# Kernel optimization log

Measured on AMD Instinct MI355X. Metric: run time of the kernel, lower is better.

The kernel has to match this reference:

```python
import jax, jax.numpy as jnp
import numpy as np

VOCAB = 10000
N_STATE = 384
N_HEAD = 6
N_CTX = 448
B = 128
T = 448  # seq len, must be <= N_CTX


def setup_inputs() -> dict:
    key = jax.random.key(0)
    ks = jax.random.split(key, 10)
    def w(k, shape, scale=0.02):
        return jax.random.normal(k, shape, dtype=jnp.float32) * scale
    return {
        "x": jax.random.randint(ks[0], (B, T), 0, VOCAB),
        "emb": w(ks[1], (VOCAB, N_STATE)),
        "Wq": w(ks[2], (N_STATE, N_STATE)), "bq": w(ks[3], (N_STATE,)),
        "Wk": w(ks[4], (N_STATE, N_STATE)),  # key layer has no bias
        "Wv": w(ks[5], (N_STATE, N_STATE)), "bv": w(ks[6], (N_STATE,)),
        "Wo": w(ks[7], (N_STATE, N_STATE)), "bo": w(ks[8], (N_STATE,)),
    }


def reference(x, emb, Wq, bq, Wk, Wv, bv, Wo, bo):
    b, t = x.shape
    d = N_STATE // N_HEAD  # 64
    scale = d ** (-0.25)

    h = emb[x]                          # [b, t, n_state] embedding lookup
    q = h @ Wq.T + bq                   # [b, t, n_state]
    k = h @ Wk.T                        # key linear has no bias
    v = h @ Wv.T + bv

    # split heads: [b, t, H, d]
    qh = q.reshape(b, t, N_HEAD, d) * scale
    kh = k.reshape(b, t, N_HEAD, d) * scale
    vh = v.reshape(b, t, N_HEAD, d)

    qk = jnp.einsum('bqhd,bkhd->bhqk', qh, kh)          # [b, H, t, t]
    mask = jnp.triu(jnp.full((t, t), -jnp.inf, dtype=qk.dtype), 1)
    qk = qk + mask                                      # causal mask add
    w = jax.nn.softmax(qk.astype(jnp.float32), axis=-1).astype(q.dtype)

    wv = jnp.einsum('bhqk,bkhd->bqhd', w, vh).reshape(b, t, N_STATE)
    out = wv @ Wo.T + bo
    return (out, k, v)
```

## Files before the change

kernel.cpp:

```cpp
#include <hip/hip_runtime.h>
#include <hip/hip_bf16.h>
#include <stdint.h>

typedef __bf16 bf16x8 __attribute__((ext_vector_type(8)));
typedef short short8v __attribute__((ext_vector_type(8)));
typedef float f32x4 __attribute__((ext_vector_type(4)));

#define B_     128
#define T_     448
#define NS     384
#define NH     6
#define HD     64
#define VOCAB_ 10000
#define NOUT   22020096

#define OFF_WQ   0
#define OFF_WK   147456
#define OFF_WV   294912
#define OFF_WO   442368
#define OFF_QTAB 589824
#define OFF_KTAB 4429824
#define OFF_VTAB 8269824
#define OFF_CTX  12109824

#define NATT (B_ * NH * 7)
#define NGAT 10752
#define NFUSE (NATT * 3)

__device__ __forceinline__ unsigned short f2bf(float f) {
    union { __bf16 h; unsigned short u; } v;
    v.h = (__bf16)f;
    return v.u;
}
__device__ __forceinline__ float bf2f(unsigned short u) {
    union { uint32_t u; float f; } v; v.u = (uint32_t)u << 16;
    return v.f;
}

__global__ __launch_bounds__(256) void k_prep(
    const float* __restrict__ Wq, const float* __restrict__ Wk,
    const float* __restrict__ Wv, const float* __restrict__ Wo,
    unsigned short* __restrict__ ws)
{
    const float* srcs[4] = {Wq, Wk, Wv, Wo};
    const int seg = blockIdx.y;
    int i = (blockIdx.x * 256 + threadIdx.x) * 4;
    if (i >= 147456) return;
    float4 v = *(const float4*)(srcs[seg] + i);
    ushort4 o;
    o.x = f2bf(v.x); o.y = f2bf(v.y); o.z = f2bf(v.z); o.w = f2bf(v.w);
    *(ushort4*)(ws + seg * 147456 + i) = o;
}

__global__ __launch_bounds__(256) void k_table(
    const float* __restrict__ emb, const unsigned short* __restrict__ ws,
    const float* __restrict__ bq, const float* __restrict__ bv,
    unsigned short* __restrict__ wso)
{
    const int p  = blockIdx.y;
    const int v0 = blockIdx.x * 32;
    const int tid = threadIdx.x;
    const int lane = tid & 63, wv = tid >> 6;

    __shared__ __align__(16) unsigned short sA[32][392];

    {
        int r = tid >> 3;
        int srow = min(v0 + r, VOCAB_ - 1);
        const float* src = emb + (size_t)srow * NS + (tid & 7) * 48;
        unsigned short* dst = &sA[r][(tid & 7) * 48];
        #pragma unroll
        for (int j = 0; j < 6; ++j) {
            float4 a0 = *(const float4*)(src + j * 8);
            float4 a1 = *(const float4*)(src + j * 8 + 4);
            ushort4 o0, o1;
            o0.x = f2bf(a0.x); o0.y = f2bf(a0.y); o0.z = f2bf(a0.z); o0.w = f2bf(a0.w);
            o1.x = f2bf(a1.x); o1.y = f2bf(a1.y); o1.z = f2bf(a1.z); o1.w = f2bf(a1.w);
            *(ushort4*)(dst + j * 8) = o0;
            *(ushort4*)(dst + j * 8 + 4) = o1;
        }
    }
    __syncthreads();

    f32x4 acc[2][6];
    #pragma unroll
    for (int i = 0; i < 2; ++i)
        #pragma unroll
        for (int j = 0; j < 6; ++j) acc[i][j] = (f32x4){0.f, 0.f, 0.f, 0.f};

    const int colA = lane & 15;
    const int kb = (lane >> 4) * 8;
    const unsigned short* wlane =
        ws + (size_t)p * 147456 + (size_t)(wv * 96 + colA) * NS + kb;

    #pragma unroll 2
    for (int kc = 0; kc < 12; ++kc) {
        bf16x8 a[2], b[6];
        #pragma unroll
        for (int mf = 0; mf < 2; ++mf)
            a[mf] = *(const bf16x8*)&sA[mf * 16 + colA][kc * 32 + kb];
        #pragma unroll
        for (int nf = 0; nf < 6; ++nf)
            b[nf] = *(const bf16x8*)(wlane + (size_t)(nf * 16) * NS + kc * 32);
        #pragma unroll
        for (int mf = 0; mf < 2; ++mf)
            #pragma unroll
            for (int nf = 0; nf < 6; ++nf)
                acc[mf][nf] = __builtin_amdgcn_mfma_f32_16x16x32_bf16(
                    a[mf], b[nf], acc[mf][nf], 0, 0, 0);
    }

    const int r0 = (lane >> 4) * 4;
    const float scale = 0.35355339059327373f;
    const float qscale = 0.35355339059327373f * 1.4426950408889634f;

    if (p == 0) {
        unsigned short* qt_ = wso + OFF_QTAB;
        #pragma unroll
        for (int nf = 0; nf < 6; ++nf) {
            int n = wv * 96 + nf * 16 + colA;
            float bias = bq[n];
            #pragma unroll
            for (int mf = 0; mf < 2; ++mf)
                #pragma unroll
                for (int r = 0; r < 4; ++r) {
                    int row = v0 + mf * 16 + r0 + r;
                    if (row < VOCAB_)
                        qt_[(size_t)row * NS + n] = f2bf((acc[mf][nf][r] + bias) * qscale);
                }
        }
    } else if (p == 1) {
        unsigned short* kt_ = wso + OFF_KTAB;
        #pragma unroll
        for (int nf = 0; nf < 6; ++nf) {
            int n = wv * 96 + nf * 16 + colA;
            #pragma unroll
            for (int mf = 0; mf < 2; ++mf)
                #pragma unroll
                for (int r = 0; r < 4; ++r) {
                    int row = v0 + mf * 16 + r0 + r;
                    if (row < VOCAB_)
                        kt_[(size_t)row * NS + n] = f2bf(acc[mf][nf][r] * scale);
                }
        }
    } else {
        unsigned short* vt_ = wso + OFF_VTAB;
        #pragma unroll
        for (int nf = 0; nf < 6; ++nf) {
            int n = wv * 96 + nf * 16 + colA;
            float bias = bv[n];
            #pragma unroll
            for (int mf = 0; mf < 2; ++mf)
                #pragma unroll
                for (int r = 0; r < 4; ++r) {
                    int row = v0 + mf * 16 + r0 + r;
                    if (row < VOCAB_)
                        vt_[(size_t)row * NS + n] = f2bf(acc[mf][nf][r] + bias);
                }
        }
    }
}

__global__ __launch_bounds__(256) void k_attn_gather(
    const int* __restrict__ x, const unsigned short* __restrict__ ws,
    unsigned short* __restrict__ ctxb,
    float* __restrict__ out_k, float* __restrict__ out_v)
{
    const int swz = (blockIdx.x & 7) * (NFUSE / 8) + (blockIdx.x >> 3);
    const int r3 = swz % 3;
    const int q3 = swz / 3;

    if (r3 != 0) {
        int i = (2 * q3 + (r3 - 1)) * 256 + threadIdx.x;
        int row = i / 48;
        int c = (i - row * 48) * 8;
        int tok = x[row];
        const unsigned short* ks = ws + OFF_KTAB + (size_t)tok * NS + c;
        const unsigned short* vs = ws + OFF_VTAB + (size_t)tok * NS + c;
        ushort4 k0 = *(const ushort4*)ks;
        ushort4 k1 = *(const ushort4*)(ks + 4);
        ushort4 v0 = *(const ushort4*)vs;
        ushort4 v1 = *(const ushort4*)(vs + 4);
        const float inv = 2.8284271247461903f;
        float4 fk0 = {bf2f(k0.x) * inv, bf2f(k0.y) * inv, bf2f(k0.z) * inv, bf2f(k0.w) * inv};
        float4 fk1 = {bf2f(k1.x) * inv, bf2f(k1.y) * inv, bf2f(k1.z) * inv, bf2f(k1.w) * inv};
        float4 fv0 = {bf2f(v0.x), bf2f(v0.y), bf2f(v0.z), bf2f(v0.w)};
        float4 fv1 = {bf2f(v1.x), bf2f(v1.y), bf2f(v1.z), bf2f(v1.w)};
        size_t base = (size_t)row * NS + c;
        *(float4*)(out_k + base)     = fk0;
        *(float4*)(out_k + base + 4) = fk1;
        *(float4*)(out_v + base)     = fv0;
        *(float4*)(out_v + base + 4) = fv1;
        return;
    }

    const int bid = q3;
    const int qt = bid % 7;
    const int h  = (bid / 7) % NH;
    const int b  = bid / (7 * NH);
    const int tid = threadIdx.x;
    const int lane = tid & 63, wv = tid >> 6;

    __shared__ __align__(16) unsigned short sK[64][72];
    __shared__ __align__(16) unsigned short sVT[64][72];
    __shared__ __align__(16) unsigned short sP[4][16][72];

    const int* xb = x + (size_t)b * T_;
    const unsigned short* qtab = ws + OFF_QTAB;
    const unsigned short* ktab = ws + OFF_KTAB;
    const unsigned short* vtab = ws + OFF_VTAB;

    const int qrow = qt * 64 + wv * 16 + (lane & 15);
    const int qtok = xb[qrow];
    const unsigned short* qbase =
        qtab + (size_t)qtok * NS + h * HD + (lane >> 4) * 8;
    bf16x8 qf0 = *(const bf16x8*)qbase;
    bf16x8 qf1 = *(const bf16x8*)(qbase + 32);

    f32x4 o[4];
    #pragma unroll
    for (int nf = 0; nf < 4; ++nf) o[nf] = (f32x4){0.f, 0.f, 0.f, 0.f};
    float lsum[4] = {0.f, 0.f, 0.f, 0.f};

    const int tk = tid >> 2;
    const int cc = (tid & 3) * 16;
    const int vd = tid & 63;
    const int vg = tid >> 6;

    short8v kr0, kr1;
    unsigned short tv[16];
    {
        int tkn = xb[tk];
        const unsigned short* kset = ktab + (size_t)tkn * NS + h * HD + cc;
        kr0 = *(const short8v*)kset;
        kr1 = *(const short8v*)(kset + 8);
        #pragma unroll
        for (int j = 0; j < 16; ++j) {
            int t = xb[vg * 16 + j];
            tv[j] = vtab[(size_t)t * NS + h * HD + vd];
        }
    }

    for (int kv = 0; kv <= qt; ++kv) {
        __syncthreads();
        *(short8v*)&sK[tk][cc]           = kr0;
        *(short8v*)&sK[tk][cc + 8]       = kr1;
        *(short8v*)&sVT[vd][vg * 16]     = *(const short8v*)&tv[0];
        *(short8v*)&sVT[vd][vg * 16 + 8] = *(const short8v*)&tv[8];
        __syncthreads();

        if (kv < qt) {
            int base = (kv + 1) * 64;
            int tkn = xb[base + tk];
            const unsigned short* kset = ktab + (size_t)tkn * NS + h * HD + cc;
            kr0 = *(const short8v*)kset;
            kr1 = *(const short8v*)(kset + 8);
            #pragma unroll
            for (int j = 0; j < 16; ++j) {
                int t = xb[base + vg * 16 + j];
                tv[j] = vtab[(size_t)t * NS + h * HD + vd];
            }
        }

        f32x4 s[4];
        #pragma unroll
        for (int nf = 0; nf < 4; ++nf) s[nf] = (f32x4){0.f, 0.f, 0.f, 0.f};
        #pragma unroll
        for (int nf = 0; nf < 4; ++nf) {
            bf16x8 kb0 = *(const bf16x8*)&sK[nf * 16 + (lane & 15)][(lane >> 4) * 8];
            s[nf] = __builtin_amdgcn_mfma_f32_16x16x32_bf16(qf0, kb0, s[nf], 0, 0, 0);
            bf16x8 kb1 = *(const bf16x8*)&sK[nf * 16 + (lane & 15)][32 + (lane >> 4) * 8];
            s[nf] = __builtin_amdgcn_mfma_f32_16x16x32_bf16(qf1, kb1, s[nf], 0, 0, 0);
        }

        if (kv == qt) {
            const int rloc = wv * 16 + (lane >> 4) * 4;
            const int cloc = lane & 15;
            #pragma unroll
            for (int nf = 0; nf < 4; ++nf)
                #pragma unroll
                for (int r = 0; r < 4; ++r) {
                    float sv = (cloc + nf * 16 > rloc + r) ? -1e30f : s[nf][r];
                    float p = exp2f(sv);
                    s[nf][r] = p;
                    lsum[r] += p;
                }
        } else {
            #pragma unroll
            for (int nf = 0; nf < 4; ++nf)
                #pragma unroll
                for (int r = 0; r < 4; ++r) {
                    float p = exp2f(s[nf][r]);
                    s[nf][r] = p;
                    lsum[r] += p;
                }
        }

        #pragma unroll
        for (int nf = 0; nf < 4; ++nf)
            #pragma unroll
            for (int r = 0; r < 4; ++r)
                sP[wv][(lane >> 4) * 4 + r][nf * 16 + (lane & 15)] = f2bf(s[nf][r]);
        asm volatile("s_waitcnt lgkmcnt(0)" ::: "memory");

        bf16x8 pa0 = *(const bf16x8*)&sP[wv][lane & 15][(lane >> 4) * 8];
        bf16x8 pa1 = *(const bf16x8*)&sP[wv][lane & 15][32 + (lane >> 4) * 8];
        #pragma unroll
        for (int nf = 0; nf < 4; ++nf) {
            bf16x8 vb0 = *(const bf16x8*)&sVT[nf * 16 + (lane & 15)][(lane >> 4) * 8];
            o[nf] = __builtin_amdgcn_mfma_f32_16x16x32_bf16(pa0, vb0, o[nf], 0, 0, 0);
            bf16x8 vb1 = *(const bf16x8*)&sVT[nf * 16 + (lane & 15)][32 + (lane >> 4) * 8];
            o[nf] = __builtin_amdgcn_mfma_f32_16x16x32_bf16(pa1, vb1, o[nf], 0, 0, 0);
        }
    }

    float inv[4];
    #pragma unroll
    for (int r = 0; r < 4; ++r) {
        float l = lsum[r];
        #pragma unroll
        for (int off = 1; off < 16; off <<= 1)
            l += __shfl_xor(l, off, 16);
        inv[r] = 1.0f / l;
    }

    #pragma unroll
    for (int nf = 0; nf < 4; ++nf) {
        int col = h * HD + nf * 16 + (lane & 15);
        #pragma unroll
        for (int r = 0; r < 4; ++r) {
            int rowg = qt * 64 + wv * 16 + (lane >> 4) * 4 + r;
            ctxb[((size_t)b * T_ + rowg) * NS + col] = f2bf(o[nf][r] * inv[r]);
        }
    }
}

__global__ __launch_bounds__(256) void k_oproj(
    const unsigned short* __restrict__ ws, const float* __restrict__ bo,
    float* __restrict__ out)
{
    const int m0 = blockIdx.x * 64;
    const int tid = threadIdx.x;
    const int lane = tid & 63, wv = tid >> 6;

    __shared__ __align__(16) unsigned short sA[64][392];

    const unsigned short* ctxb = ws + OFF_CTX;

    {
        int r = tid >> 2, seg = tid & 3;
        const unsigned short* src = ctxb + (size_t)(m0 + r) * NS + seg * 96;
        unsigned short* dst = &sA[r][seg * 96];
        #pragma unroll
        for (int j = 0; j < 12; ++j)
            *(short8v*)(dst + j * 8) = *(const short8v*)(src + j * 8);
    }
    __syncthreads();

    f32x4 acc[4][6];
    #pragma unroll
    for (int i = 0; i < 4; ++i)
        #pragma unroll
        for (int j = 0; j < 6; ++j) acc[i][j] = (f32x4){0.f, 0.f, 0.f, 0.f};

    const int colA = lane & 15;
    const int kb = (lane >> 4) * 8;
    const unsigned short* wlane =
        ws + OFF_WO + (size_t)(wv * 96 + colA) * NS + kb;

    #pragma unroll 2
    for (int kc = 0; kc < 12; ++kc) {
        bf16x8 a[4], bfr[6];
        #pragma unroll
        for (int mf = 0; mf < 4; ++mf)
            a[mf] = *(const bf16x8*)&sA[mf * 16 + colA][kc * 32 + kb];
        #pragma unroll
        for (int nf = 0; nf < 6; ++nf)
            bfr[nf] = *(const bf16x8*)(wlane + (size_t)(nf * 16) * NS + kc * 32);
        #pragma unroll
        for (int mf = 0; mf < 4; ++mf)
            #pragma unroll
            for (int nf = 0; nf < 6; ++nf)
                acc[mf][nf] = __builtin_amdgcn_mfma_f32_16x16x32_bf16(
                    a[mf], bfr[nf], acc[mf][nf], 0, 0, 0);
    }

    const int r0 = (lane >> 4) * 4;
    #pragma unroll
    for (int nf = 0; nf < 6; ++nf) {
        int n = wv * 96 + nf * 16 + colA;
        float bias = bo[n];
        #pragma unroll
        for (int mf = 0; mf < 4; ++mf)
            #pragma unroll
            for (int r = 0; r < 4; ++r)
                out[(size_t)(m0 + mf * 16 + r0 + r) * NS + n] = acc[mf][nf][r] + bias;
    }
}

extern "C" void kernel_launch(void* const* d_in, const int* in_sizes, int n_in,
                              void* d_out, int out_size, void* d_ws, size_t ws_size,
                              hipStream_t stream) {
    const int*   x   = (const int*)d_in[0];
    const float* emb = (const float*)d_in[1];
    const float* Wq  = (const float*)d_in[2];
    const float* bq  = (const float*)d_in[3];
    const float* Wk  = (const float*)d_in[4];
    const float* Wv  = (const float*)d_in[5];
    const float* bv  = (const float*)d_in[6];
    const float* Wo  = (const float*)d_in[7];
    const float* bo  = (const float*)d_in[8];

    float* out   = (float*)d_out;
    float* out_k = out + NOUT;
    float* out_v = out + 2 * (size_t)NOUT;
    unsigned short* ws = (unsigned short*)d_ws;

    k_prep<<<dim3(144, 4), 256, 0, stream>>>(Wq, Wk, Wv, Wo, ws);
    k_table<<<dim3(313, 3), 256, 0, stream>>>(emb, ws, bq, bv, ws);
    k_attn_gather<<<dim3(NFUSE), 256, 0, stream>>>(x, ws, ws + OFF_CTX,
                                                   out_k, out_v);
    k_oproj<<<dim3(896), 256, 0, stream>>>(ws, bo, out);
}
```

Baseline: 192.9 us.

## Fuse output projection into attention blocks looping over all heads

Each attention block now handles one batch and query tile across all six heads sequentially. It writes the normalized context into shared memory and then runs the Wo projection directly. This removes the bf16 context round-trip through global memory and the separate oproj launch. The cost is far fewer attention blocks (896 instead of 5376) doing longer serial work, plus about 50KB more shared memory per block, which can reduce occupancy and load balance. Query tiles are now scheduled longest-first.

```diff
diff --git a/kernel.cpp b/kernel.cpp
--- a/kernel.cpp
+++ b/kernel.cpp
@@ -21,11 +21,10 @@
 #define OFF_QTAB 589824
 #define OFF_KTAB 4429824
 #define OFF_VTAB 8269824
-#define OFF_CTX  12109824
-
-#define NATT (B_ * NH * 7)
-#define NGAT 10752
-#define NFUSE (NATT * 3)
+
+#define NATT2  896
+#define NGAT   10752
+#define NFUSE  (NATT2 + NGAT)
 
 __device__ __forceinline__ unsigned short f2bf(float f) {
     union { __bf16 h; unsigned short u; } v;
@@ -161,17 +160,18 @@
     }
 }
 
-__global__ __launch_bounds__(256) void k_attn_gather(
+__global__ __launch_bounds__(256) void k_fused(
     const int* __restrict__ x, const unsigned short* __restrict__ ws,
-    unsigned short* __restrict__ ctxb,
+    const float* __restrict__ bo, float* __restrict__ out,
     float* __restrict__ out_k, float* __restrict__ out_v)
 {
-    const int swz = (blockIdx.x & 7) * (NFUSE / 8) + (blockIdx.x >> 3);
-    const int r3 = swz % 3;
-    const int q3 = swz / 3;
-
-    if (r3 != 0) {
-        int i = (2 * q3 + (r3 - 1)) * 256 + threadIdx.x;
+    const int gid = blockIdx.x;
+    const int tid = threadIdx.x;
+
+    if (gid >= NATT2) {
+        int g = gid - NATT2;
+        int cs = (g & 7) * (NGAT / 8) + (g >> 3);
+        int i = cs * 256 + tid;
         int row = i / 48;
         int c = (i - row * 48) * 8;
         int tok = x[row];
@@ -194,16 +194,15 @@
         return;
     }
 
-    const int bid = q3;
-    const int qt = bid % 7;
-    const int h  = (bid / 7) % NH;
-    const int b  = bid / (7 * NH);
-    const int tid = threadIdx.x;
+    const int as = (gid & 7) * (NATT2 / 8) + (gid >> 3);
+    const int b  = as / 7;
+    const int qt = 6 - (as % 7);
     const int lane = tid & 63, wv = tid >> 6;
 
     __shared__ __align__(16) unsigned short sK[64][72];
     __shared__ __align__(16) unsigned short sVT[64][72];
     __shared__ __align__(16) unsigned short sP[4][16][72];
+    __shared__ __align__(16) unsigned short sO[64][392];
 
     const int* xb = x + (size_t)b * T_;
     const unsigned short* qtab = ws + OFF_QTAB;
@@ -212,15 +211,12 @@
 
     const int qrow = qt * 64 + wv * 16 + (lane & 15);
     const int qtok = xb[qrow];
-    const unsigned short* qbase =
-        qtab + (size_t)qtok * NS + h * HD + (lane >> 4) * 8;
-    bf16x8 qf0 = *(const bf16x8*)qbase;
-    bf16x8 qf1 = *(const bf16x8*)(qbase + 32);
 
     f32x4 o[4];
     #pragma unroll
     for (int nf = 0; nf < 4; ++nf) o[nf] = (f32x4){0.f, 0.f, 0.f, 0.f};
     float lsum[4] = {0.f, 0.f, 0.f, 0.f};
+    bf16x8 qf0, qf1;
 
     const int tk = tid >> 2;
     const int cc = (tid & 3) * 16;
@@ -231,17 +227,19 @@
     unsigned short tv[16];
     {
         int tkn = xb[tk];
-        const unsigned short* kset = ktab + (size_t)tkn * NS + h * HD + cc;
+        const unsigned short* kset = ktab + (size_t)tkn * NS + cc;
         kr0 = *(const short8v*)kset;
         kr1 = *(const short8v*)(kset + 8);
         #pragma unroll
         for (int j = 0; j < 16; ++j) {
             int t = xb[vg * 16 + j];
-            tv[j] = vtab[(size_t)t * NS + h * HD + vd];
-        }
-    }
-
-    for (int kv = 0; kv <= qt; ++kv) {
+            tv[j] = vtab[(size_t)t * NS + vd];
+        }
+    }
+
+    int h = 0, kv = 0;
+    const int NT = NH * (qt + 1);
+    for (int t = 0; t < NT; ++t) {
         __syncthreads();
         *(short8v*)&sK[tk][cc]           = kr0;
         *(short8v*)&sK[tk][cc + 8]       = kr1;
@@ -249,17 +247,28 @@
         *(short8v*)&sVT[vd][vg * 16 + 8] = *(const short8v*)&tv[8];
         __syncthreads();
 
-        if (kv < qt) {
-            int base = (kv + 1) * 64;
-            int tkn = xb[base + tk];
-            const unsigned short* kset = ktab + (size_t)tkn * NS + h * HD + cc;
-            kr0 = *(const short8v*)kset;
-            kr1 = *(const short8v*)(kset + 8);
-            #pragma unroll
-            for (int j = 0; j < 16; ++j) {
-                int t = xb[base + vg * 16 + j];
-                tv[j] = vtab[(size_t)t * NS + h * HD + vd];
+        {
+            int nh = h, nkv = kv + 1;
+            if (nkv > qt) { nkv = 0; nh++; }
+            if (nh < NH) {
+                int base = nkv * 64;
+                int tkn = xb[base + tk];
+                const unsigned short* kset = ktab + (size_t)tkn * NS + nh * HD + cc;
+                kr0 = *(const short8v*)kset;
+                kr1 = *(const short8v*)(kset + 8);
+                #pragma unroll
+                for (int j = 0; j < 16; ++j) {
+                    int tt = xb[base + vg * 16 + j];
+                    tv[j] = vtab[(size_t)tt * NS + nh * HD + vd];
+                }
             }
+        }
+
+        if (kv == 0) {
+            const unsigned short* qbase =
+                qtab + (size_t)qtok * NS + h * HD + (lane >> 4) * 8;
+            qf0 = *(const bf16x8*)qbase;
+            qf1 = *(const bf16x8*)(qbase + 32);
         }
 
         f32x4 s[4];
@@ -312,49 +321,34 @@
             bf16x8 vb1 = *(const bf16x8*)&sVT[nf * 16 + (lane & 15)][32 + (lane >> 4) * 8];
             o[nf] = __builtin_amdgcn_mfma_f32_16x16x32_bf16(pa1, vb1, o[nf], 0, 0, 0);
         }
-    }
-
-    float inv[4];
-    #pragma unroll
-    for (int r = 0; r < 4; ++r) {
-        float l = lsum[r];
-        #pragma unroll
-        for (int off = 1; off < 16; off <<= 1)
-            l += __shfl_xor(l, off, 16);
-        inv[r] = 1.0f / l;
-    }
-
-    #pragma unroll
-    for (int nf = 0; nf < 4; ++nf) {
-        int col = h * HD + nf * 16 + (lane & 15);
-        #pragma unroll
-        for (int r = 0; r < 4; ++r) {
-            int rowg = qt * 64 + wv * 16 + (lane >> 4) * 4 + r;
-            ctxb[((size_t)b * T_ + rowg) * NS + col] = f2bf(o[nf][r] * inv[r]);
-        }
-    }
-}
-
-__global__ __launch_bounds__(256) void k_oproj(
-    const unsigned short* __restrict__ ws, const float* __restrict__ bo,
-    float* __restrict__ out)
-{
-    const int m0 = blockIdx.x * 64;
-    const int tid = threadIdx.x;
-    const int lane = tid & 63, wv = tid >> 6;
-
-    __shared__ __align__(16) unsigned short sA[64][392];
-
-    const unsigned short* ctxb = ws + OFF_CTX;
-
-    {
-        int r = tid >> 2, seg = tid & 3;
-        const unsigned short* src = ctxb + (size_t)(m0 + r) * NS + seg * 96;
-        unsigned short* dst = &sA[r][seg * 96];
-        #pragma unroll
-        for (int j = 0; j < 12; ++j)
-            *(short8v*)(dst + j * 8) = *(const short8v*)(src + j * 8);
-    }
+
+        if (kv == qt) {
+            float inv[4];
+            #pragma unroll
+            for (int r = 0; r < 4; ++r) {
+                float l = lsum[r];
+                #pragma unroll
+                for (int off = 1; off < 16; off <<= 1)
+                    l += __shfl_xor(l, off, 16);
+                inv[r] = 1.0f / l;
+            }
+            #pragma unroll
+            for (int nf = 0; nf < 4; ++nf) {
+                int col = h * HD + nf * 16 + (lane & 15);
+                #pragma unroll
+                for (int r = 0; r < 4; ++r)
+                    sO[wv * 16 + (lane >> 4) * 4 + r][col] = f2bf(o[nf][r] * inv[r]);
+            }
+            #pragma unroll
+            for (int nf = 0; nf < 4; ++nf) o[nf] = (f32x4){0.f, 0.f, 0.f, 0.f};
+            #pragma unroll
+            for (int r = 0; r < 4; ++r) lsum[r] = 0.f;
+            h++; kv = 0;
+        } else {
+            kv++;
+        }
+    }
+
     __syncthreads();
 
     f32x4 acc[4][6];
@@ -373,7 +367,7 @@
         bf16x8 a[4], bfr[6];
         #pragma unroll
         for (int mf = 0; mf < 4; ++mf)
-            a[mf] = *(const bf16x8*)&sA[mf * 16 + colA][kc * 32 + kb];
+            a[mf] = *(const bf16x8*)&sO[mf * 16 + colA][kc * 32 + kb];
         #pragma unroll
         for (int nf = 0; nf < 6; ++nf)
             bfr[nf] = *(const bf16x8*)(wlane + (size_t)(nf * 16) * NS + kc * 32);
@@ -385,6 +379,7 @@
                     a[mf], bfr[nf], acc[mf][nf], 0, 0, 0);
     }
 
+    const int m0 = b * T_ + qt * 64;
     const int r0 = (lane >> 4) * 4;
     #pragma unroll
     for (int nf = 0; nf < 6; ++nf) {
@@ -418,7 +413,5 @@
 
     k_prep<<<dim3(144, 4), 256, 0, stream>>>(Wq, Wk, Wv, Wo, ws);
     k_table<<<dim3(313, 3), 256, 0, stream>>>(emb, ws, bq, bv, ws);
-    k_attn_gather<<<dim3(NFUSE), 256, 0, stream>>>(x, ws, ws + OFF_CTX,
-                                                   out_k, out_v);
-    k_oproj<<<dim3(896), 256, 0, stream>>>(ws, bo, out);
-}
+    k_fused<<<dim3(NFUSE), 256, 0, stream>>>(x, ws, bo, out, out_k, out_v);
+}
```

After: 293.7 us. +52.3%, slower.

## Split gather from attention and materialize contiguous bf16 K/V buffers

Applied to the files above, without the earlier changes.

The fused attention+gather kernel becomes two kernels. The gather kernel now also writes bf16 K and V into per-batch contiguous buffers, and the attention kernel reads those buffers directly instead of doing indirect token-indexed lookups into the vocab tables. This removes the dependent index loads and scattered reads from the attention inner loop. The cost is an extra kernel launch, roughly 45 MB of additional bf16 writes and reads, and the loss of overlap between gather and attention work.

```diff
diff --git a/kernel.cpp b/kernel.cpp
--- a/kernel.cpp
+++ b/kernel.cpp
@@ -21,11 +21,12 @@
 #define OFF_QTAB 589824
 #define OFF_KTAB 4429824
 #define OFF_VTAB 8269824
-#define OFF_CTX  12109824
+#define OFF_KB   12109824
+#define OFF_VB   34129920
+#define OFF_CTX  56150016
 
 #define NATT (B_ * NH * 7)
 #define NGAT 10752
-#define NFUSE (NATT * 3)
 
 __device__ __forceinline__ unsigned short f2bf(float f) {
     union { __bf16 h; unsigned short u; } v;
@@ -161,43 +162,45 @@
     }
 }
 
-__global__ __launch_bounds__(256) void k_attn_gather(
+__global__ __launch_bounds__(256) void k_gather(
     const int* __restrict__ x, const unsigned short* __restrict__ ws,
-    unsigned short* __restrict__ ctxb,
-    float* __restrict__ out_k, float* __restrict__ out_v)
+    float* __restrict__ out_k, float* __restrict__ out_v,
+    unsigned short* __restrict__ kbuf, unsigned short* __restrict__ vbuf)
 {
-    const int swz = (blockIdx.x & 7) * (NFUSE / 8) + (blockIdx.x >> 3);
-    const int r3 = swz % 3;
-    const int q3 = swz / 3;
-
-    if (r3 != 0) {
-        int i = (2 * q3 + (r3 - 1)) * 256 + threadIdx.x;
-        int row = i / 48;
-        int c = (i - row * 48) * 8;
-        int tok = x[row];
-        const unsigned short* ks = ws + OFF_KTAB + (size_t)tok * NS + c;
-        const unsigned short* vs = ws + OFF_VTAB + (size_t)tok * NS + c;
-        ushort4 k0 = *(const ushort4*)ks;
-        ushort4 k1 = *(const ushort4*)(ks + 4);
-        ushort4 v0 = *(const ushort4*)vs;
-        ushort4 v1 = *(const ushort4*)(vs + 4);
-        const float inv = 2.8284271247461903f;
-        float4 fk0 = {bf2f(k0.x) * inv, bf2f(k0.y) * inv, bf2f(k0.z) * inv, bf2f(k0.w) * inv};
-        float4 fk1 = {bf2f(k1.x) * inv, bf2f(k1.y) * inv, bf2f(k1.z) * inv, bf2f(k1.w) * inv};
-        float4 fv0 = {bf2f(v0.x), bf2f(v0.y), bf2f(v0.z), bf2f(v0.w)};
-        float4 fv1 = {bf2f(v1.x), bf2f(v1.y), bf2f(v1.z), bf2f(v1.w)};
-        size_t base = (size_t)row * NS + c;
-        *(float4*)(out_k + base)     = fk0;
-        *(float4*)(out_k + base + 4) = fk1;
-        *(float4*)(out_v + base)     = fv0;
-        *(float4*)(out_v + base + 4) = fv1;
-        return;
-    }
-
-    const int bid = q3;
-    const int qt = bid % 7;
-    const int h  = (bid / 7) % NH;
-    const int b  = bid / (7 * NH);
+    int i = blockIdx.x * 256 + threadIdx.x;
+    int row = i / 48;
+    int c = (i - row * 48) * 8;
+    int tok = x[row];
+    const unsigned short* ks = ws + OFF_KTAB + (size_t)tok * NS + c;
+    const unsigned short* vs = ws + OFF_VTAB + (size_t)tok * NS + c;
+    ushort4 k0 = *(const ushort4*)ks;
+    ushort4 k1 = *(const ushort4*)(ks + 4);
+    ushort4 v0 = *(const ushort4*)vs;
+    ushort4 v1 = *(const ushort4*)(vs + 4);
+    size_t bb = (size_t)row * NS + c;
+    *(ushort4*)(kbuf + bb)     = k0;
+    *(ushort4*)(kbuf + bb + 4) = k1;
+    *(ushort4*)(vbuf + bb)     = v0;
+    *(ushort4*)(vbuf + bb + 4) = v1;
+    const float inv = 2.8284271247461903f;
+    float4 fk0 = {bf2f(k0.x) * inv, bf2f(k0.y) * inv, bf2f(k0.z) * inv, bf2f(k0.w) * inv};
+    float4 fk1 = {bf2f(k1.x) * inv, bf2f(k1.y) * inv, bf2f(k1.z) * inv, bf2f(k1.w) * inv};
+    float4 fv0 = {bf2f(v0.x), bf2f(v0.y), bf2f(v0.z), bf2f(v0.w)};
+    float4 fv1 = {bf2f(v1.x), bf2f(v1.y), bf2f(v1.z), bf2f(v1.w)};
+    *(float4*)(out_k + bb)     = fk0;
+    *(float4*)(out_k + bb + 4) = fk1;
+    *(float4*)(out_v + bb)     = fv0;
+    *(float4*)(out_v + bb + 4) = fv1;
+}
+
+__global__ __launch_bounds__(256) void k_attn(
+    const int* __restrict__ x, const unsigned short* __restrict__ ws,
+    unsigned short* __restrict__ ctxb)
+{
+    const int as = (blockIdx.x & 7) * (NATT / 8) + (blockIdx.x >> 3);
+    const int b  = as / 42;
+    const int h  = (as / 7) % NH;
+    const int qt = as % 7;
     const int tid = threadIdx.x;
     const int lane = tid & 63, wv = tid >> 6;
 
@@ -207,8 +210,8 @@
 
     const int* xb = x + (size_t)b * T_;
     const unsigned short* qtab = ws + OFF_QTAB;
-    const unsigned short* ktab = ws + OFF_KTAB;
-    const unsigned short* vtab = ws + OFF_VTAB;
+    const unsigned short* kb_ = ws + OFF_KB + (size_t)b * T_ * NS + h * HD;
+    const unsigned short* vb_ = ws + OFF_VB + (size_t)b * T_ * NS + h * HD;
 
     const int qrow = qt * 64 + wv * 16 + (lane & 15);
     const int qtok = xb[qrow];
@@ -230,15 +233,12 @@
     short8v kr0, kr1;
     unsigned short tv[16];
     {
-        int tkn = xb[tk];
-        const unsigned short* kset = ktab + (size_t)tkn * NS + h * HD + cc;
+        const unsigned short* kset = kb_ + (size_t)tk * NS + cc;
         kr0 = *(const short8v*)kset;
         kr1 = *(const short8v*)(kset + 8);
         #pragma unroll
-        for (int j = 0; j < 16; ++j) {
-            int t = xb[vg * 16 + j];
-            tv[j] = vtab[(size_t)t * NS + h * HD + vd];
-        }
+        for (int j = 0; j < 16; ++j)
+            tv[j] = vb_[(size_t)(vg * 16 + j) * NS + vd];
     }
 
     for (int kv = 0; kv <= qt; ++kv) {
@@ -251,15 +251,12 @@
 
         if (kv < qt) {
             int base = (kv + 1) * 64;
-            int tkn = xb[base + tk];
-            const unsigned short* kset = ktab + (size_t)tkn * NS + h * HD + cc;
+            const unsigned short* kset = kb_ + (size_t)(base + tk) * NS + cc;
             kr0 = *(const short8v*)kset;
             kr1 = *(const short8v*)(kset + 8);
             #pragma unroll
-            for (int j = 0; j < 16; ++j) {
-                int t = xb[base + vg * 16 + j];
-                tv[j] = vtab[(size_t)t * NS + h * HD + vd];
-            }
+            for (int j = 0; j < 16; ++j)
+                tv[j] = vb_[(size_t)(base + vg * 16 + j) * NS + vd];
         }
 
         f32x4 s[4];
@@ -418,7 +415,8 @@
 
     k_prep<<<dim3(144, 4), 256, 0, stream>>>(Wq, Wk, Wv, Wo, ws);
     k_table<<<dim3(313, 3), 256, 0, stream>>>(emb, ws, bq, bv, ws);
-    k_attn_gather<<<dim3(NFUSE), 256, 0, stream>>>(x, ws, ws + OFF_CTX,
-                                                   out_k, out_v);
+    k_gather<<<dim3(NGAT), 256, 0, stream>>>(x, ws, out_k, out_v,
+                                             ws + OFF_KB, ws + OFF_VB);
+    k_attn<<<dim3(NATT), 256, 0, stream>>>(x, ws, ws + OFF_CTX);
     k_oproj<<<dim3(896), 256, 0, stream>>>(ws, bo, out);
 }
```

Result: slower. 228.0 us (+18.2%).

## Pair causal query tiles per 512-thread block to share K/V tile loads

Applied to the files above, without the earlier changes.

The fused attention and K/V gather kernel now uses 512-thread blocks in which two 64-row query tiles (2p and 2p+1) of the same batch/head share each staged K/V tile, with the last tile (6) running alone on half the waves. Waves whose query tile is past the current KV block skip compute, and the gather blocks now cover 512 elements each. This cuts redundant K/V gathering and LDS staging across query tiles and halves the attention block count. In exchange, the lower-tile waves sit idle on the final KV iteration, the lone-tile blocks leave four waves unused, and the per-block LDS grows with the larger sP buffer.

```diff
diff --git a/kernel.cpp b/kernel.cpp
--- a/kernel.cpp
+++ b/kernel.cpp
@@ -23,9 +23,9 @@
 #define OFF_VTAB 8269824
 #define OFF_CTX  12109824
 
-#define NATT (B_ * NH * 7)
-#define NGAT 10752
-#define NFUSE (NATT * 3)
+#define NATT3  3072
+#define NGAT2  5376
+#define NFUSE2 (NATT3 + NGAT2)
 
 __device__ __forceinline__ unsigned short f2bf(float f) {
     union { __bf16 h; unsigned short u; } v;
@@ -161,17 +161,18 @@
     }
 }
 
-__global__ __launch_bounds__(256) void k_attn_gather(
+__global__ __launch_bounds__(512, 4) void k_fused(
     const int* __restrict__ x, const unsigned short* __restrict__ ws,
     unsigned short* __restrict__ ctxb,
     float* __restrict__ out_k, float* __restrict__ out_v)
 {
-    const int swz = (blockIdx.x & 7) * (NFUSE / 8) + (blockIdx.x >> 3);
-    const int r3 = swz % 3;
-    const int q3 = swz / 3;
-
-    if (r3 != 0) {
-        int i = (2 * q3 + (r3 - 1)) * 256 + threadIdx.x;
+    const int gid = blockIdx.x;
+    const int tid = threadIdx.x;
+
+    if (gid >= NATT3) {
+        int g = gid - NATT3;
+        int cs = (g & 7) * (NGAT2 / 8) + (g >> 3);
+        int i = cs * 512 + tid;
         int row = i / 48;
         int c = (i - row * 48) * 8;
         int tok = x[row];
@@ -194,23 +195,29 @@
         return;
     }
 
-    const int bid = q3;
-    const int qt = bid % 7;
-    const int h  = (bid / 7) % NH;
-    const int b  = bid / (7 * NH);
-    const int tid = threadIdx.x;
-    const int lane = tid & 63, wv = tid >> 6;
+    const int as = (gid & 7) * (NATT3 / 8) + (gid >> 3);
+    const int b  = as / 24;
+    const int h  = (as >> 2) % NH;
+    const int pr = as & 3;
+    const int qta = pr * 2;
+    const bool lone = (pr == 3);
+    const int kvmax = lone ? 6 : qta + 1;
+
+    const int lane = tid & 63, w = tid >> 6;
+    const int sub = w & 3;
+    const int qt_w = lone ? 6 : (qta + (w >> 2));
+    const bool active = (!lone) || (w < 4);
 
     __shared__ __align__(16) unsigned short sK[64][72];
     __shared__ __align__(16) unsigned short sVT[64][72];
-    __shared__ __align__(16) unsigned short sP[4][16][72];
+    __shared__ __align__(16) unsigned short sP[8][16][72];
 
     const int* xb = x + (size_t)b * T_;
     const unsigned short* qtab = ws + OFF_QTAB;
     const unsigned short* ktab = ws + OFF_KTAB;
     const unsigned short* vtab = ws + OFF_VTAB;
 
-    const int qrow = qt * 64 + wv * 16 + (lane & 15);
+    const int qrow = qt_w * 64 + sub * 16 + (lane & 15);
     const int qtok = xb[qrow];
     const unsigned short* qbase =
         qtab + (size_t)qtok * NS + h * HD + (lane >> 4) * 8;
@@ -222,115 +229,114 @@
     for (int nf = 0; nf < 4; ++nf) o[nf] = (f32x4){0.f, 0.f, 0.f, 0.f};
     float lsum[4] = {0.f, 0.f, 0.f, 0.f};
 
-    const int tk = tid >> 2;
-    const int cc = (tid & 3) * 16;
+    const int tk = tid >> 3;
+    const int cc = (tid & 7) * 8;
     const int vd = tid & 63;
     const int vg = tid >> 6;
 
-    short8v kr0, kr1;
-    unsigned short tv[16];
+    short8v kr;
+    unsigned short tv[8];
     {
         int tkn = xb[tk];
-        const unsigned short* kset = ktab + (size_t)tkn * NS + h * HD + cc;
-        kr0 = *(const short8v*)kset;
-        kr1 = *(const short8v*)(kset + 8);
-        #pragma unroll
-        for (int j = 0; j < 16; ++j) {
-            int t = xb[vg * 16 + j];
+        kr = *(const short8v*)(ktab + (size_t)tkn * NS + h * HD + cc);
+        #pragma unroll
+        for (int j = 0; j < 8; ++j) {
+            int t = xb[vg * 8 + j];
             tv[j] = vtab[(size_t)t * NS + h * HD + vd];
         }
     }
 
-    for (int kv = 0; kv <= qt; ++kv) {
+    for (int kv = 0; kv <= kvmax; ++kv) {
         __syncthreads();
-        *(short8v*)&sK[tk][cc]           = kr0;
-        *(short8v*)&sK[tk][cc + 8]       = kr1;
-        *(short8v*)&sVT[vd][vg * 16]     = *(const short8v*)&tv[0];
-        *(short8v*)&sVT[vd][vg * 16 + 8] = *(const short8v*)&tv[8];
+        *(short8v*)&sK[tk][cc]      = kr;
+        *(short8v*)&sVT[vd][vg * 8] = *(const short8v*)&tv[0];
         __syncthreads();
 
-        if (kv < qt) {
+        if (kv < kvmax) {
             int base = (kv + 1) * 64;
             int tkn = xb[base + tk];
-            const unsigned short* kset = ktab + (size_t)tkn * NS + h * HD + cc;
-            kr0 = *(const short8v*)kset;
-            kr1 = *(const short8v*)(kset + 8);
-            #pragma unroll
-            for (int j = 0; j < 16; ++j) {
-                int t = xb[base + vg * 16 + j];
+            kr = *(const short8v*)(ktab + (size_t)tkn * NS + h * HD + cc);
+            #pragma unroll
+            for (int j = 0; j < 8; ++j) {
+                int t = xb[base + vg * 8 + j];
                 tv[j] = vtab[(size_t)t * NS + h * HD + vd];
             }
         }
 
-        f32x4 s[4];
-        #pragma unroll
-        for (int nf = 0; nf < 4; ++nf) s[nf] = (f32x4){0.f, 0.f, 0.f, 0.f};
+        const bool doQK = active && (kv <= qt_w);
+        if (doQK) {
+            f32x4 s[4];
+            #pragma unroll
+            for (int nf = 0; nf < 4; ++nf) s[nf] = (f32x4){0.f, 0.f, 0.f, 0.f};
+            #pragma unroll
+            for (int nf = 0; nf < 4; ++nf) {
+                bf16x8 kb0 = *(const bf16x8*)&sK[nf * 16 + (lane & 15)][(lane >> 4) * 8];
+                s[nf] = __builtin_amdgcn_mfma_f32_16x16x32_bf16(qf0, kb0, s[nf], 0, 0, 0);
+                bf16x8 kb1 = *(const bf16x8*)&sK[nf * 16 + (lane & 15)][32 + (lane >> 4) * 8];
+                s[nf] = __builtin_amdgcn_mfma_f32_16x16x32_bf16(qf1, kb1, s[nf], 0, 0, 0);
+            }
+
+            if (kv == qt_w) {
+                const int rloc = sub * 16 + (lane >> 4) * 4;
+                const int cloc = lane & 15;
+                #pragma unroll
+                for (int nf = 0; nf < 4; ++nf)
+                    #pragma unroll
+                    for (int r = 0; r < 4; ++r) {
+                        float sv = (cloc + nf * 16 > rloc + r) ? -1e30f : s[nf][r];
+                        float p = exp2f(sv);
+                        s[nf][r] = p;
+                        lsum[r] += p;
+                    }
+            } else {
+                #pragma unroll
+                for (int nf = 0; nf < 4; ++nf)
+                    #pragma unroll
+                    for (int r = 0; r < 4; ++r) {
+                        float p = exp2f(s[nf][r]);
+                        s[nf][r] = p;
+                        lsum[r] += p;
+                    }
+            }
+
+            #pragma unroll
+            for (int nf = 0; nf < 4; ++nf)
+                #pragma unroll
+                for (int r = 0; r < 4; ++r)
+                    sP[w][(lane >> 4) * 4 + r][nf * 16 + (lane & 15)] = f2bf(s[nf][r]);
+            asm volatile("s_waitcnt lgkmcnt(0)" ::: "memory");
+
+            bf16x8 pa0 = *(const bf16x8*)&sP[w][lane & 15][(lane >> 4) * 8];
+            bf16x8 pa1 = *(const bf16x8*)&sP[w][lane & 15][32 + (lane >> 4) * 8];
+            #pragma unroll
+            for (int nf = 0; nf < 4; ++nf) {
+                bf16x8 vb0 = *(const bf16x8*)&sVT[nf * 16 + (lane & 15)][(lane >> 4) * 8];
+                o[nf] = __builtin_amdgcn_mfma_f32_16x16x32_bf16(pa0, vb0, o[nf], 0, 0, 0);
+                bf16x8 vb1 = *(const bf16x8*)&sVT[nf * 16 + (lane & 15)][32 + (lane >> 4) * 8];
+                o[nf] = __builtin_amdgcn_mfma_f32_16x16x32_bf16(pa1, vb1, o[nf], 0, 0, 0);
+            }
+        }
+    }
+
+    if (active) {
+        float inv[4];
+        #pragma unroll
+        for (int r = 0; r < 4; ++r) {
+            float l = lsum[r];
+            #pragma unroll
+            for (int off = 1; off < 16; off <<= 1)
+                l += __shfl_xor(l, off, 16);
+            inv[r] = 1.0f / l;
+        }
+
         #pragma unroll
         for (int nf = 0; nf < 4; ++nf) {
-            bf16x8 kb0 = *(const bf16x8*)&sK[nf * 16 + (lane & 15)][(lane >> 4) * 8];
-            s[nf] = __builtin_amdgcn_mfma_f32_16x16x32_bf16(qf0, kb0, s[nf], 0, 0, 0);
-            bf16x8 kb1 = *(const bf16x8*)&sK[nf * 16 + (lane & 15)][32 + (lane >> 4) * 8];
-            s[nf] = __builtin_amdgcn_mfma_f32_16x16x32_bf16(qf1, kb1, s[nf], 0, 0, 0);
-        }
-
-        if (kv == qt) {
-            const int rloc = wv * 16 + (lane >> 4) * 4;
-            const int cloc = lane & 15;
-            #pragma unroll
-            for (int nf = 0; nf < 4; ++nf)
-                #pragma unroll
-                for (int r = 0; r < 4; ++r) {
-                    float sv = (cloc + nf * 16 > rloc + r) ? -1e30f : s[nf][r];
-                    float p = exp2f(sv);
-                    s[nf][r] = p;
-                    lsum[r] += p;
-                }
-        } else {
-            #pragma unroll
-            for (int nf = 0; nf < 4; ++nf)
-                #pragma unroll
-                for (int r = 0; r < 4; ++r) {
-                    float p = exp2f(s[nf][r]);
-                    s[nf][r] = p;
-                    lsum[r] += p;
-                }
-        }
-
-        #pragma unroll
-        for (int nf = 0; nf < 4; ++nf)
-            #pragma unroll
-            for (int r = 0; r < 4; ++r)
-                sP[wv][(lane >> 4) * 4 + r][nf * 16 + (lane & 15)] = f2bf(s[nf][r]);
-        asm volatile("s_waitcnt lgkmcnt(0)" ::: "memory");
-
-        bf16x8 pa0 = *(const bf16x8*)&sP[wv][lane & 15][(lane >> 4) * 8];
-        bf16x8 pa1 = *(const bf16x8*)&sP[wv][lane & 15][32 + (lane >> 4) * 8];
-        #pragma unroll
-        for (int nf = 0; nf < 4; ++nf) {
-            bf16x8 vb0 = *(const bf16x8*)&sVT[nf * 16 + (lane & 15)][(lane >> 4) * 8];
-            o[nf] = __builtin_amdgcn_mfma_f32_16x16x32_bf16(pa0, vb0, o[nf], 0, 0, 0);
-            bf16x8 vb1 = *(const bf16x8*)&sVT[nf * 16 + (lane & 15)][32 + (lane >> 4) * 8];
-            o[nf] = __builtin_amdgcn_mfma_f32_16x16x32_bf16(pa1, vb1, o[nf], 0, 0, 0);
-        }
-    }
-
-    float inv[4];
-    #pragma unroll
-    for (int r = 0; r < 4; ++r) {
-        float l = lsum[r];
-        #pragma unroll
-        for (int off = 1; off < 16; off <<= 1)
-            l += __shfl_xor(l, off, 16);
-        inv[r] = 1.0f / l;
-    }
-
-    #pragma unroll
-    for (int nf = 0; nf < 4; ++nf) {
-        int col = h * HD + nf * 16 + (lane & 15);
-        #pragma unroll
-        for (int r = 0; r < 4; ++r) {
-            int rowg = qt * 64 + wv * 16 + (lane >> 4) * 4 + r;
-            ctxb[((size_t)b * T_ + rowg) * NS + col] = f2bf(o[nf][r] * inv[r]);
+            int col = h * HD + nf * 16 + (lane & 15);
+            #pragma unroll
+            for (int r = 0; r < 4; ++r) {
+                int rowg = qt_w * 64 + sub * 16 + (lane >> 4) * 4 + r;
+                ctxb[((size_t)b * T_ + rowg) * NS + col] = f2bf(o[nf][r] * inv[r]);
+            }
         }
     }
 }
@@ -418,7 +424,7 @@
 
     k_prep<<<dim3(144, 4), 256, 0, stream>>>(Wq, Wk, Wv, Wo, ws);
     k_table<<<dim3(313, 3), 256, 0, stream>>>(emb, ws, bq, bv, ws);
-    k_attn_gather<<<dim3(NFUSE), 256, 0, stream>>>(x, ws, ws + OFF_CTX,
-                                                   out_k, out_v);
+    k_fused<<<dim3(NFUSE2), 512, 0, stream>>>(x, ws, ws + OFF_CTX,
+                                              out_k, out_v);
     k_oproj<<<dim3(896), 256, 0, stream>>>(ws, bo, out);
 }
```

Measured after the change: 220.9 us. +14.5%, slower.
